# Performance work log

Hardware: AMD Instinct MI355X
Metric: run time of the kernel (lower is better)

Reference implementation:

```python
import jax, jax.numpy as jnp
import numpy as np

H = 8  # heads

def setup_inputs() -> dict:
    key = jax.random.key(0)
    k0, k1, k2, k3 = jax.random.split(key, 4)
    B, L, D = 4, 1024, 512
    K = jax.random.normal(k0, (B, L, D), dtype=jnp.float32)
    Q = jax.random.normal(k1, (B, L, D), dtype=jnp.float32)
    V = jax.random.normal(k2, (B, L, D), dtype=jnp.float32)
    # realistic padding: each doc has a valid length in [L/2, L]
    lengths = jax.random.randint(k3, (B,), L // 2, L + 1)
    pos = jnp.arange(L)
    valid = pos[None, :] < lengths[:, None]          # [B, L]
    pad_mask = valid[:, :, None] & valid[:, None, :]  # [B, L, L]
    bx_packed = ~valid                                # [B, L] True where padded
    doc_sizes = lengths.astype(jnp.float32)[:, None]  # [B, 1]
    gamma = jnp.ones((H,), dtype=jnp.float32)   # LayerNorm(heads) weight
    beta = jnp.zeros((H,), dtype=jnp.float32)   # LayerNorm(heads) bias
    return {"K": K, "Q": Q, "V": V, "doc_sizes": doc_sizes,
            "gamma": gamma, "beta": beta,
            "pad_mask": pad_mask, "bx_packed": bx_packed}


def reference(K, Q, V, doc_sizes, gamma, beta, pad_mask, bx_packed):
    B, L, D = K.shape
    d = D // H
    split = lambda x: x.reshape(B, L, H, d).transpose(0, 2, 1, 3)  # [B,H,L,d]
    k, q, v = split(K), split(Q), split(V)

    # InnerMatrix: inner-product similarity -> [B,H,L,L]
    cw = jnp.einsum('bhld,bhmd->bhlm', k, q)

    # LayerNorm over heads axis (torch views [B,H,L*L] -> [B,L*L,H], LN over H)
    mu = cw.mean(axis=1, keepdims=True)
    var = cw.var(axis=1, keepdims=True)
    cw = (cw - mu) / jnp.sqrt(var + 1e-5)
    cw = cw * gamma[None, :, None, None] + beta[None, :, None, None]
    # leaky = -1.0 default: float(leaky > 0) == 0, leaky-relu branch is a no-op

    # masked softmax over keys, NaN (fully-masked rows) -> 0
    cw = jnp.where(pad_mask[:, None, :, :], cw, -jnp.inf)
    cw = jax.nn.softmax(cw, axis=-1)
    cw = jnp.where(jnp.isnan(cw), 0.0, cw)

    # aggregated per-token weights: sum over queries, mean over heads -> [B,L]
    w = cw.sum(axis=-2).mean(axis=1)
    w = w / doc_sizes
    w = jnp.where(bx_packed, -jnp.inf, w)
    w = jax.nn.softmax(w, axis=-1)
    w = jnp.where(jnp.isnan(w), 0.0, w)

    # weighted V aggregation, merge heads back -> [B,L,D]
    out = jnp.einsum('bhlm,bhmd->bhld', cw, v)
    out = out.transpose(0, 2, 1, 3).reshape(B, L, D)
    return out, w[..., None]
```

## Files before the change

kernel.cpp:

```cpp
#include <hip/hip_runtime.h>
#include <math.h>

#define L_ 1024
#define D_ 512

typedef _Float16 half8 __attribute__((ext_vector_type(8)));
typedef _Float16 half4v __attribute__((ext_vector_type(4)));
typedef _Float16 half2v __attribute__((ext_vector_type(2)));
typedef float floatx4 __attribute__((ext_vector_type(4)));

__global__ __launch_bounds__(256) void prep(
    const float* __restrict__ K, const float* __restrict__ Q,
    const float* __restrict__ V,
    _Float16* __restrict__ K16, _Float16* __restrict__ Q16,
    _Float16* __restrict__ Vt)
{
    __shared__ _Float16 tile[64][72];
    const int t = threadIdx.x;
    const int bi = blockIdx.x;
    if (bi < 256) {
        for (int it = 0; it < 16; ++it) {
            size_t f = (size_t)bi * 4096 + it * 256 + t;
            const float4* src; _Float16* dst;
            if (f < 524288) { src = (const float4*)K; dst = K16; }
            else            { src = (const float4*)Q; dst = Q16; f -= 524288; }
            float4 v = src[f];
            half4v h = { (_Float16)v.x, (_Float16)v.y, (_Float16)v.z, (_Float16)v.w };
            *(half4v*)&dst[f * 4] = h;
        }
    } else {
        const int id = bi - 256;
        const int mt = id & 15, h = (id >> 4) & 7, b = id >> 7;
        const float4* Vf4 = (const float4*)V;
        for (int it = 0; it < 4; ++it) {
            const int ml = (t >> 4) + 16 * it;
            const int c4 = t & 15;
            float4 v = Vf4[(size_t)(b * 1024 + mt * 64 + ml) * 128 + h * 16 + c4];
            tile[c4 * 4 + 0][ml] = (_Float16)v.x;
            tile[c4 * 4 + 1][ml] = (_Float16)v.y;
            tile[c4 * 4 + 2][ml] = (_Float16)v.z;
            tile[c4 * 4 + 3][ml] = (_Float16)v.w;
        }
        __syncthreads();
        const int d = t >> 2, seg = t & 3;
        half8 o0 = *(half8*)&tile[d][seg * 16];
        half8 o1 = *(half8*)&tile[d][seg * 16 + 8];
        size_t obase = ((size_t)(b * 8 + h) * 64 + d) * 1024 + mt * 64 + seg * 16;
        *(half8*)&Vt[obase] = o0;
        *(half8*)&Vt[obase + 8] = o1;
    }
}

__global__ __launch_bounds__(256) void qk_ln(
    const _Float16* __restrict__ K16, const _Float16* __restrict__ Q16,
    const float* __restrict__ gamma, const float* __restrict__ beta,
    const float* __restrict__ doc,
    _Float16* __restrict__ S, float* __restrict__ spart)
{
    __shared__ _Float16 se[2][128][66];

    const int t  = threadIdx.x;
    const int bi = blockIdx.x;
    const int b  = bi & 3;
    const int lt = (bi >> 2) & 63;
    const int q  = bi >> 8;
    const int wv = t >> 6, lane = t & 63;
    const int col = lane & 15, quad = lane >> 4;
    const int len = (int)doc[b];
    const int lbase = lt * 16;

    float g[8], be[8], M = 0.f;
    #pragma unroll
    for (int h = 0; h < 8; ++h) {
        g[h] = gamma[h]; be[h] = beta[h];
        M = fmaxf(M, 2.8285f * fabsf(g[h]) + fabsf(be[h]));
    }

    const _Float16* Kb = K16 + (size_t)b * 524288;
    const _Float16* Qb = Q16 + (size_t)b * 524288;
    const size_t krow = (size_t)(lbase + col) * 512;

    half8 a0[8], a1[8];
    #pragma unroll
    for (int h = 0; h < 8; ++h) {
        a0[h] = *(const half8*)&Kb[krow + h * 64 + quad * 8];
        a1[h] = *(const half8*)&Kb[krow + h * 64 + 32 + quad * 8];
    }

    float sum[8][4];
    #pragma unroll
    for (int h = 0; h < 8; ++h)
        #pragma unroll
        for (int r = 0; r < 4; ++r) sum[h][r] = 0.f;

    for (int mt = 0; mt < 4; ++mt) {
        const int m0 = q * 256 + mt * 64 + wv * 16;
        const size_t qrow = (size_t)(m0 + col) * 512;
        floatx4 c[8];
        #pragma unroll
        for (int h = 0; h < 8; ++h) {
            half8 b0 = *(const half8*)&Qb[qrow + h * 64 + quad * 8];
            half8 b1 = *(const half8*)&Qb[qrow + h * 64 + 32 + quad * 8];
            floatx4 z = {0.f, 0.f, 0.f, 0.f};
            z    = __builtin_amdgcn_mfma_f32_16x16x32_f16(a0[h], b0, z, 0, 0, 0);
            c[h] = __builtin_amdgcn_mfma_f32_16x16x32_f16(a1[h], b1, c[h] = z, 0, 0, 0);
        }
        const bool mok = (m0 + col) < len;
        #pragma unroll
        for (int r = 0; r < 4; ++r) {
            const int l = lbase + quad * 4 + r;
            float mu = 0.f;
            #pragma unroll
            for (int h = 0; h < 8; ++h) mu += c[h][r];
            mu *= 0.125f;
            float var = 0.f;
            #pragma unroll
            for (int h = 0; h < 8; ++h) { float dd = c[h][r] - mu; var += dd * dd; }
            var *= 0.125f;
            const float rs = 1.0f / sqrtf(var + 1e-5f);
            const bool keep = mok && (l < len);
            #pragma unroll
            for (int h = 0; h < 8; ++h) {
                float e = 0.f;
                if (keep) {
                    float val = (c[h][r] - mu) * rs * g[h] + be[h];
                    e = __expf(val - M);
                }
                sum[h][r] += e;
                se[mt & 1][h * 16 + quad * 4 + r][wv * 16 + col] = (_Float16)e;
            }
        }
        __syncthreads();
        const int mbase = q * 256 + mt * 64;
        #pragma unroll
        for (int it = 0; it < 4; ++it) {
            const int row = it * 32 + (t >> 3);
            const int h = row >> 4, l = row & 15;
            half8 v = *(half8*)&se[mt & 1][row][(t & 7) * 8];
            *(half8*)&S[((size_t)((b * 8 + h) * 1024 + lbase + l)) * 1024
                        + mbase + (t & 7) * 8] = v;
        }
    }

    #pragma unroll
    for (int h = 0; h < 8; ++h)
        #pragma unroll
        for (int r = 0; r < 4; ++r) {
            float s = sum[h][r];
            s += __shfl_xor(s, 1); s += __shfl_xor(s, 2);
            s += __shfl_xor(s, 4); s += __shfl_xor(s, 8);
            sum[h][r] = s;
        }
    if (col == 0) {
        #pragma unroll
        for (int h = 0; h < 8; ++h)
            #pragma unroll
            for (int r = 0; r < 4; ++r)
                spart[((size_t)((b * 8 + h) * 1024 + lbase + quad * 4 + r)) * 16
                      + q * 4 + wv] = sum[h][r];
    }
}

__global__ __launch_bounds__(256) void stats_reduce(
    const float* __restrict__ spart, const float* __restrict__ doc,
    float* __restrict__ inv)
{
    const int i = blockIdx.x * 256 + threadIdx.x;
    const int l = i & 1023;
    const int b = i >> 13;
    const int len = (int)doc[b];
    float s = 0.f;
    #pragma unroll
    for (int j = 0; j < 16; ++j) s += spart[(size_t)i * 16 + j];
    inv[i] = (l < len && s > 0.f) ? 1.0f / s : 0.f;
}

__global__ __launch_bounds__(256) void pv(
    const _Float16* __restrict__ S, const _Float16* __restrict__ Vt,
    const float* __restrict__ invp,
    float* __restrict__ out)
{
    const int t = threadIdx.x, wv = t >> 6, lane = t & 63;
    const int col = lane & 15, quad = lane >> 4;
    const int bi = blockIdx.x;
    const int lb = bi & 15, h = (bi >> 4) & 7, b = bi >> 7;
    const int l0 = lb * 64 + wv * 16;

    const _Float16* Arow = S + ((size_t)(b * 8 + h) * 1024 + l0 + col) * 1024;
    const _Float16* Vb = Vt + (size_t)(b * 8 + h) * 65536;

    floatx4 acc[4] = {{0,0,0,0},{0,0,0,0},{0,0,0,0},{0,0,0,0}};

    half8 ebuf[8];
    #pragma unroll
    for (int i = 0; i < 8; ++i)
        ebuf[i] = *(const half8*)&Arow[i * 32 + quad * 8];

    #pragma unroll
    for (int kc = 0; kc < 32; ++kc) {
        half8 a = ebuf[kc & 7];
        if (kc + 8 < 32)
            ebuf[kc & 7] = *(const half8*)&Arow[(kc + 8) * 32 + quad * 8];
        #pragma unroll
        for (int dt = 0; dt < 4; ++dt) {
            half8 bf = *(const half8*)&Vb[(size_t)(dt * 16 + col) * 1024
                                          + kc * 32 + quad * 8];
            acc[dt] = __builtin_amdgcn_mfma_f32_16x16x32_f16(a, bf, acc[dt], 0, 0, 0);
        }
    }

    #pragma unroll
    for (int r = 0; r < 4; ++r) {
        const int l = l0 + quad * 4 + r;
        const float ivr = invp[(size_t)(b * 8 + h) * 1024 + l];
        float* orow = out + (size_t)(b * 1024 + l) * 512 + h * 64;
        #pragma unroll
        for (int dt = 0; dt < 4; ++dt)
            orow[dt * 16 + col] = acc[dt][r] * ivr;
    }
}

__global__ __launch_bounds__(256) void wsum(
    const _Float16* __restrict__ S, const float* __restrict__ invp,
    float* __restrict__ wacc)
{
    const int t = threadIdx.x;
    const int bi = blockIdx.x;
    const int lc = bi & 15, h = (bi >> 4) & 7, b = bi >> 7;
    const size_t rbase = (size_t)(b * 8 + h) * 1024 + lc * 64;
    const _Float16* Sb = S + rbase * 1024;
    const float* ivb = invp + rbase;
    const int m0 = t * 4;

    float a0 = 0.f, a1 = 0.f, a2 = 0.f, a3 = 0.f;
    #pragma unroll 8
    for (int l = 0; l < 64; ++l) {
        const float iv = ivb[l];
        half4v e = *(const half4v*)&Sb[(size_t)l * 1024 + m0];
        a0 += (float)e[0] * iv;
        a1 += (float)e[1] * iv;
        a2 += (float)e[2] * iv;
        a3 += (float)e[3] * iv;
    }
    float* wb = wacc + b * 1024 + m0;
    atomicAdd(&wb[0], a0);
    atomicAdd(&wb[1], a1);
    atomicAdd(&wb[2], a2);
    atomicAdd(&wb[3], a3);
}

__global__ __launch_bounds__(256) void w_final(
    const float* __restrict__ wacc, const float* __restrict__ doc,
    float* __restrict__ wout)
{
    const int b = blockIdx.x;
    const int t = threadIdx.x;
    __shared__ float red[4];

    const float ds = doc[b];
    const int len = (int)ds;

    float v[4];
    float mx = -INFINITY;
    #pragma unroll
    for (int i = 0; i < 4; ++i) {
        const int m = t + 256 * i;
        const float raw = wacc[b * L_ + m];
        v[i] = (m < len) ? (raw * 0.125f) / ds : -INFINITY;
        mx = fmaxf(mx, v[i]);
    }
    #pragma unroll
    for (int off = 1; off < 64; off <<= 1) mx = fmaxf(mx, __shfl_xor(mx, off));
    if ((t & 63) == 0) red[t >> 6] = mx;
    __syncthreads();
    mx = fmaxf(fmaxf(red[0], red[1]), fmaxf(red[2], red[3]));

    float e[4];
    float sm = 0.f;
    #pragma unroll
    for (int i = 0; i < 4; ++i) {
        e[i] = (v[i] != -INFINITY) ? __expf(v[i] - mx) : 0.f;
        sm += e[i];
    }
    #pragma unroll
    for (int off = 1; off < 64; off <<= 1) sm += __shfl_xor(sm, off);
    __syncthreads();
    if ((t & 63) == 0) red[t >> 6] = sm;
    __syncthreads();
    sm = red[0] + red[1] + red[2] + red[3];
    const float inv = (sm > 0.f) ? 1.0f / sm : 0.f;

    #pragma unroll
    for (int i = 0; i < 4; ++i)
        wout[b * L_ + t + 256 * i] = e[i] * inv;
}

extern "C" void kernel_launch(void* const* d_in, const int* in_sizes, int n_in,
                              void* d_out, int out_size, void* d_ws, size_t ws_size,
                              hipStream_t stream)
{
    const float* K     = (const float*)d_in[0];
    const float* Q     = (const float*)d_in[1];
    const float* V     = (const float*)d_in[2];
    const float* doc   = (const float*)d_in[3];
    const float* gamma = (const float*)d_in[4];
    const float* beta  = (const float*)d_in[5];

    float* out  = (float*)d_out;
    float* wout = out + (size_t)4 * L_ * D_;

    _Float16* S    = (_Float16*)d_ws;
    _Float16* K16  = S + (size_t)33554432;
    _Float16* Q16  = K16 + 2097152;
    _Float16* Vt   = Q16 + 2097152;
    float*    spart = (float*)(Vt + 2097152);
    float*    invp  = spart + 524288;
    float*    wacc  = invp + 32768;

    hipMemsetAsync(wacc, 0, 4096 * sizeof(float), stream);
    prep        <<<dim3(768),  dim3(256), 0, stream>>>(K, Q, V, K16, Q16, Vt);
    qk_ln       <<<dim3(1024), dim3(256), 0, stream>>>(K16, Q16, gamma, beta, doc, S, spart);
    stats_reduce<<<dim3(128),  dim3(256), 0, stream>>>(spart, doc, invp);
    pv          <<<dim3(512),  dim3(256), 0, stream>>>(S, Vt, invp, out);
    wsum        <<<dim3(512),  dim3(256), 0, stream>>>(S, invp, wacc);
    w_final     <<<dim3(4),    dim3(256), 0, stream>>>(wacc, doc, wout);
}
```

Baseline: 214.3 us.

## Store S in 16x16 tiled layout so qk_ln writes directly without LDS

The attention-probability matrix S is changed from row-major [L][L] to a tiled layout of 16-column m-tiles, with swapped MFMA operands so each lane holds four consecutive m values for one l row. qk_ln can then write half4 vectors straight to global memory, dropping the shared-memory staging buffer and the barrier. pv and wsum are rewritten to read the new layout, and wsum now reduces with shuffles before the atomics. K fragments are reloaded per m-tile instead of kept in registers, which lowers register pressure at the cost of extra loads. The prep kernel's grid is split into more, smaller blocks.

Result: faster. 207.7 us (-3.1%).

```diff
diff --git a/kernel.cpp b/kernel.cpp
--- a/kernel.cpp
+++ b/kernel.cpp
@@ -8,6 +8,7 @@
 typedef _Float16 half4v __attribute__((ext_vector_type(4)));
 typedef _Float16 half2v __attribute__((ext_vector_type(2)));
 typedef float floatx4 __attribute__((ext_vector_type(4)));
+
 
 __global__ __launch_bounds__(256) void prep(
     const float* __restrict__ K, const float* __restrict__ Q,
@@ -18,9 +19,9 @@
     __shared__ _Float16 tile[64][72];
     const int t = threadIdx.x;
     const int bi = blockIdx.x;
-    if (bi < 256) {
-        for (int it = 0; it < 16; ++it) {
-            size_t f = (size_t)bi * 4096 + it * 256 + t;
+    if (bi < 512) {
+        for (int it = 0; it < 8; ++it) {
+            size_t f = (size_t)bi * 2048 + it * 256 + t;
             const float4* src; _Float16* dst;
             if (f < 524288) { src = (const float4*)K; dst = K16; }
             else            { src = (const float4*)Q; dst = Q16; f -= 524288; }
@@ -29,7 +30,7 @@
             *(half4v*)&dst[f * 4] = h;
         }
     } else {
-        const int id = bi - 256;
+        const int id = bi - 512;
         const int mt = id & 15, h = (id >> 4) & 7, b = id >> 7;
         const float4* Vf4 = (const float4*)V;
         for (int it = 0; it < 4; ++it) {
@@ -57,8 +58,6 @@
     const float* __restrict__ doc,
     _Float16* __restrict__ S, float* __restrict__ spart)
 {
-    __shared__ _Float16 se[2][128][66];
-
     const int t  = threadIdx.x;
     const int bi = blockIdx.x;
     const int b  = bi & 3;
@@ -79,36 +78,30 @@
     const _Float16* Kb = K16 + (size_t)b * 524288;
     const _Float16* Qb = Q16 + (size_t)b * 524288;
     const size_t krow = (size_t)(lbase + col) * 512;
-
-    half8 a0[8], a1[8];
-    #pragma unroll
-    for (int h = 0; h < 8; ++h) {
-        a0[h] = *(const half8*)&Kb[krow + h * 64 + quad * 8];
-        a1[h] = *(const half8*)&Kb[krow + h * 64 + 32 + quad * 8];
-    }
-
-    float sum[8][4];
-    #pragma unroll
-    for (int h = 0; h < 8; ++h)
-        #pragma unroll
-        for (int r = 0; r < 4; ++r) sum[h][r] = 0.f;
-
+    const bool lok = (lbase + col) < len;
+
+    float sum[8];
+    #pragma unroll
+    for (int h = 0; h < 8; ++h) sum[h] = 0.f;
+
+    #pragma unroll
     for (int mt = 0; mt < 4; ++mt) {
-        const int m0 = q * 256 + mt * 64 + wv * 16;
-        const size_t qrow = (size_t)(m0 + col) * 512;
+        const int mstart = q * 256 + mt * 64 + wv * 16;
+        const size_t qrow = (size_t)(mstart + col) * 512;
         floatx4 c[8];
         #pragma unroll
         for (int h = 0; h < 8; ++h) {
-            half8 b0 = *(const half8*)&Qb[qrow + h * 64 + quad * 8];
-            half8 b1 = *(const half8*)&Qb[qrow + h * 64 + 32 + quad * 8];
+            half8 qa0 = *(const half8*)&Qb[qrow + h * 64 + quad * 8];
+            half8 qa1 = *(const half8*)&Qb[qrow + h * 64 + 32 + quad * 8];
+            half8 kb0 = *(const half8*)&Kb[krow + h * 64 + quad * 8];
+            half8 kb1 = *(const half8*)&Kb[krow + h * 64 + 32 + quad * 8];
             floatx4 z = {0.f, 0.f, 0.f, 0.f};
-            z    = __builtin_amdgcn_mfma_f32_16x16x32_f16(a0[h], b0, z, 0, 0, 0);
-            c[h] = __builtin_amdgcn_mfma_f32_16x16x32_f16(a1[h], b1, c[h] = z, 0, 0, 0);
-        }
-        const bool mok = (m0 + col) < len;
+            z    = __builtin_amdgcn_mfma_f32_16x16x32_f16(qa0, kb0, z, 0, 0, 0);
+            c[h] = __builtin_amdgcn_mfma_f32_16x16x32_f16(qa1, kb1, z, 0, 0, 0);
+        }
+        half4v ev[8];
         #pragma unroll
         for (int r = 0; r < 4; ++r) {
-            const int l = lbase + quad * 4 + r;
             float mu = 0.f;
             #pragma unroll
             for (int h = 0; h < 8; ++h) mu += c[h][r];
@@ -118,46 +111,34 @@
             for (int h = 0; h < 8; ++h) { float dd = c[h][r] - mu; var += dd * dd; }
             var *= 0.125f;
             const float rs = 1.0f / sqrtf(var + 1e-5f);
-            const bool keep = mok && (l < len);
+            const bool keep = lok && (mstart + quad * 4 + r) < len;
             #pragma unroll
             for (int h = 0; h < 8; ++h) {
                 float e = 0.f;
-                if (keep) {
-                    float val = (c[h][r] - mu) * rs * g[h] + be[h];
-                    e = __expf(val - M);
-                }
-                sum[h][r] += e;
-                se[mt & 1][h * 16 + quad * 4 + r][wv * 16 + col] = (_Float16)e;
+                if (keep) e = __expf((c[h][r] - mu) * rs * g[h] + be[h] - M);
+                sum[h] += e;
+                ev[h][r] = (_Float16)e;
             }
         }
-        __syncthreads();
-        const int mbase = q * 256 + mt * 64;
-        #pragma unroll
-        for (int it = 0; it < 4; ++it) {
-            const int row = it * 32 + (t >> 3);
-            const int h = row >> 4, l = row & 15;
-            half8 v = *(half8*)&se[mt & 1][row][(t & 7) * 8];
-            *(half8*)&S[((size_t)((b * 8 + h) * 1024 + lbase + l)) * 1024
-                        + mbase + (t & 7) * 8] = v;
-        }
-    }
-
-    #pragma unroll
-    for (int h = 0; h < 8; ++h)
-        #pragma unroll
-        for (int r = 0; r < 4; ++r) {
-            float s = sum[h][r];
-            s += __shfl_xor(s, 1); s += __shfl_xor(s, 2);
-            s += __shfl_xor(s, 4); s += __shfl_xor(s, 8);
-            sum[h][r] = s;
-        }
-    if (col == 0) {
+        const int mtile = q * 16 + mt * 4 + wv;
+        #pragma unroll
+        for (int h = 0; h < 8; ++h) {
+            *(half4v*)&S[((size_t)((b * 8 + h) * 64 + mtile)) * 16384
+                         + (size_t)(lbase + col) * 16 + quad * 4] = ev[h];
+        }
+    }
+
+    #pragma unroll
+    for (int h = 0; h < 8; ++h) {
+        float s = sum[h];
+        s += __shfl_xor(s, 16); s += __shfl_xor(s, 32);
+        sum[h] = s;
+    }
+    if (quad == 0) {
         #pragma unroll
         for (int h = 0; h < 8; ++h)
-            #pragma unroll
-            for (int r = 0; r < 4; ++r)
-                spart[((size_t)((b * 8 + h) * 1024 + lbase + quad * 4 + r)) * 16
-                      + q * 4 + wv] = sum[h][r];
+            spart[((size_t)((b * 8 + h) * 1024 + lbase + col)) * 16 + q * 4 + wv] =
+                sum[h];
     }
 }
 
@@ -186,7 +167,9 @@
     const int lb = bi & 15, h = (bi >> 4) & 7, b = bi >> 7;
     const int l0 = lb * 64 + wv * 16;
 
-    const _Float16* Arow = S + ((size_t)(b * 8 + h) * 1024 + l0 + col) * 1024;
+    const int q2 = quad >> 1;
+    const size_t abase = (size_t)(b * 8 + h) * 1048576
+                       + (size_t)(l0 + col) * 16 + (quad & 1) * 8;
     const _Float16* Vb = Vt + (size_t)(b * 8 + h) * 65536;
 
     floatx4 acc[4] = {{0,0,0,0},{0,0,0,0},{0,0,0,0},{0,0,0,0}};
@@ -194,13 +177,13 @@
     half8 ebuf[8];
     #pragma unroll
     for (int i = 0; i < 8; ++i)
-        ebuf[i] = *(const half8*)&Arow[i * 32 + quad * 8];
+        ebuf[i] = *(const half8*)&S[abase + (size_t)(i * 2 + q2) * 16384];
 
     #pragma unroll
     for (int kc = 0; kc < 32; ++kc) {
         half8 a = ebuf[kc & 7];
         if (kc + 8 < 32)
-            ebuf[kc & 7] = *(const half8*)&Arow[(kc + 8) * 32 + quad * 8];
+            ebuf[kc & 7] = *(const half8*)&S[abase + (size_t)((kc + 8) * 2 + q2) * 16384];
         #pragma unroll
         for (int dt = 0; dt < 4; ++dt) {
             half8 bf = *(const half8*)&Vb[(size_t)(dt * 16 + col) * 1024
@@ -224,29 +207,41 @@
     const _Float16* __restrict__ S, const float* __restrict__ invp,
     float* __restrict__ wacc)
 {
-    const int t = threadIdx.x;
+    const int t = threadIdx.x, lane = t & 63;
     const int bi = blockIdx.x;
-    const int lc = bi & 15, h = (bi >> 4) & 7, b = bi >> 7;
-    const size_t rbase = (size_t)(b * 8 + h) * 1024 + lc * 64;
-    const _Float16* Sb = S + rbase * 1024;
-    const float* ivb = invp + rbase;
-    const int m0 = t * 4;
-
-    float a0 = 0.f, a1 = 0.f, a2 = 0.f, a3 = 0.f;
-    #pragma unroll 8
-    for (int l = 0; l < 64; ++l) {
-        const float iv = ivb[l];
-        half4v e = *(const half4v*)&Sb[(size_t)l * 1024 + m0];
-        a0 += (float)e[0] * iv;
-        a1 += (float)e[1] * iv;
-        a2 += (float)e[2] * iv;
-        a3 += (float)e[3] * iv;
-    }
-    float* wb = wacc + b * 1024 + m0;
-    atomicAdd(&wb[0], a0);
-    atomicAdd(&wb[1], a1);
-    atomicAdd(&wb[2], a2);
-    atomicAdd(&wb[3], a3);
+    const int tg = bi & 15, h = (bi >> 4) & 7, b = bi >> 7;
+    const int tile = tg * 4 + (t >> 6);
+    const int loff = lane >> 1, hi = lane & 1;
+    const _Float16* Sb = S + ((size_t)((b * 8 + h) * 64 + tile)) * 16384 + hi * 8;
+    const float* ivb = invp + (size_t)(b * 8 + h) * 1024;
+
+    float acc[8];
+    #pragma unroll
+    for (int j = 0; j < 8; ++j) acc[j] = 0.f;
+
+    for (int l0 = 0; l0 < 1024; l0 += 128) {
+        #pragma unroll
+        for (int u = 0; u < 4; ++u) {
+            const int l = l0 + u * 32 + loff;
+            const float iv = ivb[l];
+            half8 e = *(const half8*)&Sb[(size_t)l * 16];
+            #pragma unroll
+            for (int j = 0; j < 8; ++j) acc[j] += (float)e[j] * iv;
+        }
+    }
+    #pragma unroll
+    for (int j = 0; j < 8; ++j) {
+        float s = acc[j];
+        s += __shfl_xor(s, 2);  s += __shfl_xor(s, 4);
+        s += __shfl_xor(s, 8);  s += __shfl_xor(s, 16);
+        s += __shfl_xor(s, 32);
+        acc[j] = s;
+    }
+    if (lane < 2) {
+        float* wb = wacc + b * 1024 + tile * 16 + hi * 8;
+        #pragma unroll
+        for (int j = 0; j < 8; ++j) atomicAdd(&wb[j], acc[j]);
+    }
 }
 
 __global__ __launch_bounds__(256) void w_final(
@@ -318,7 +313,7 @@
     float*    wacc  = invp + 32768;
 
     hipMemsetAsync(wacc, 0, 4096 * sizeof(float), stream);
-    prep        <<<dim3(768),  dim3(256), 0, stream>>>(K, Q, V, K16, Q16, Vt);
+    prep        <<<dim3(1024), dim3(256), 0, stream>>>(K, Q, V, K16, Q16, Vt);
     qk_ln       <<<dim3(1024), dim3(256), 0, stream>>>(K16, Q16, gamma, beta, doc, S, spart);
     stats_reduce<<<dim3(128),  dim3(256), 0, stream>>>(spart, doc, invp);
     pv          <<<dim3(512),  dim3(256), 0, stream>>>(S, Vt, invp, out);
```
